# Kernel tuning notes

Hardware: AMD Instinct MI355X
Metric: run time of the kernel (lower is better)

Reference implementation:

```python
import jax, jax.numpy as jnp
import numpy as np

N, C, T, V = 32, 96, 256, 25
S, REL, OUT, BC, KS = 3, 12, 96, 24, 5
DILS = (1, 2)


def setup_inputs() -> dict:
    key = jax.random.key(0)
    ks = jax.random.split(key, 32)
    rn = lambda i, sh, s=1.0: jax.random.normal(ks[i], sh, dtype=jnp.float32) * s
    ru = lambda i, sh: jax.random.uniform(ks[i], sh, dtype=jnp.float32, minval=0.5, maxval=1.5)
    return dict(
        x=rn(0, (N, C, T, V)),
        spd_A=rn(1, (V, V), 0.1),
        A3=rn(2, (S, V, V), 0.1),
        A6=rn(3, (6, V, V), 0.1),
        alpha=jnp.array([0.5], jnp.float32),
        beta=jnp.array([0.5], jnp.float32),
        gamma=jnp.array([0.5], jnp.float32),
        c1_w=rn(4, (S, REL, C), 0.1), c1_b=rn(5, (S, REL), 0.1),
        c2_w=rn(6, (S, REL, C), 0.1), c2_b=rn(7, (S, REL), 0.1),
        c4_w=rn(8, (S, OUT, REL), 0.1), c4_b=rn(9, (S, OUT), 0.1),
        c3_w=rn(10, (S, OUT, C), 0.1), c3_b=rn(11, (S, OUT), 0.1),
        gbn_s=ru(12, (OUT,)), gbn_b=rn(13, (OUT,), 0.1),
        pw_w=rn(14, (4, BC, OUT), 0.1), pw_b=rn(15, (4, BC), 0.1),
        pwbn_s=ru(16, (4, BC)), pwbn_b=rn(17, (4, BC), 0.1),
        tc_w=rn(18, (2, BC, BC, KS), 0.1), tc_b=rn(19, (2, BC), 0.1),
        tcbn_s=ru(20, (2, BC)), tcbn_b=rn(21, (2, BC), 0.1),
        mpbn_s=ru(22, (BC,)), mpbn_b=rn(23, (BC,), 0.1),
    )


def _bn4(h, s, b):  # eval-mode BN folded to per-channel scale/shift, h: [N,C,T,V]
    return h * s[None, :, None, None] + b[None, :, None, None]


def reference(x, spd_A, A3, A6, alpha, beta, gamma,
              c1_w, c1_b, c2_w, c2_b, c4_w, c4_b, c3_w, c3_b,
              gbn_s, gbn_b, pw_w, pw_b, pwbn_s, pwbn_b,
              tc_w, tc_b, tcbn_s, tcbn_b, mpbn_s, mpbn_b):
    # ---- unit_gcn with CTRGC relation modeling ----
    xm = x.mean(axis=2)                                           # [N,C,V] (1x1 conv commutes with T-mean)
    x1 = jnp.einsum('ncv,src->nsrv', xm, c1_w) + c1_b[None, :, :, None]
    x2 = jnp.einsum('ncv,src->nsrv', xm, c2_w) + c2_b[None, :, :, None]
    R = jnp.tanh(x1[..., :, None] - x2[..., None, :])             # [N,S,REL,V,V]
    M = jnp.einsum('nsruv,sor->nsouv', R, c4_w) + c4_b[None, :, :, None, None]
    A6_ex = jnp.tile(A6, (OUT // 6, 1, 1))                        # [OUT,V,V]; A6_ex[c] = A6[c % 6]
    A_at = (M * alpha[0] + A3[None, :, None] + A6_ex[None, None] * beta[0]
            + spd_A * gamma[0])                                   # [N,S,OUT,V,V]
    y = jnp.zeros((N, OUT, T, V), x.dtype)
    for s_ in range(S):
        x3 = jnp.einsum('nctv,oc->notv', x, c3_w[s_]) + c3_b[s_][None, :, None, None]
        y = y + jnp.einsum('nouv,notv->notu', A_at[:, s_], x3)
    y = jax.nn.relu(_bn4(y, gbn_s, gbn_b) + x)                    # residual down = identity (in==out)
    # ---- MultiScale_TemporalConv (internal residual=False) ----
    outs = []
    for b in range(2):  # dilated temporal branches
        h = jax.nn.relu(_bn4(jnp.einsum('nctv,oc->notv', y, pw_w[b])
                             + pw_b[b][None, :, None, None], pwbn_s[b], pwbn_b[b]))
        d = DILS[b]
        pad = 2 * d  # (KS + (KS-1)*(d-1) - 1)//2 for KS=5
        h = jax.lax.conv_general_dilated(
            h, tc_w[b][..., None], window_strides=(1, 1),
            padding=[(pad, pad), (0, 0)], rhs_dilation=(d, 1),
            dimension_numbers=('NCHW', 'OIHW', 'NCHW')) + tc_b[b][None, :, None, None]
        outs.append(_bn4(h, tcbn_s[b], tcbn_b[b]))
    # max-pool branch
    h = jax.nn.relu(_bn4(jnp.einsum('nctv,oc->notv', y, pw_w[2])
                         + pw_b[2][None, :, None, None], pwbn_s[2], pwbn_b[2]))
    h = jax.lax.reduce_window(h, -jnp.inf, jax.lax.max, (1, 1, 3, 1), (1, 1, 1, 1),
                              [(0, 0), (0, 0), (1, 1), (0, 0)])
    outs.append(_bn4(h, mpbn_s, mpbn_b))
    # plain 1x1 branch
    h = jnp.einsum('nctv,oc->notv', y, pw_w[3]) + pw_b[3][None, :, None, None]
    outs.append(_bn4(h, pwbn_s[3], pwbn_b[3]))
    out = jnp.concatenate(outs, axis=1)                           # [N,OUT,T,V]
    return jax.nn.relu(out + x)                                   # outer residual = identity
```

## Files before the change

### kernel.cpp

```cpp
#include <hip/hip_runtime.h>
#include <hip/hip_bf16.h>

typedef __hip_bfloat16 bf16;
typedef __attribute__((ext_vector_type(4))) _Float16 half4;
typedef __attribute__((ext_vector_type(2))) _Float16 half2v;
typedef __attribute__((ext_vector_type(4))) float f32x4;

#define NN 32
#define CC 96
#define TT 256
#define VV 25
#define SS 3
#define RR 12
#define OO 96
#define BCC 24
#define TV (TT*VV)
#define VV2 (VV*VV)

__device__ __forceinline__ float b2f(bf16 v){ return __bfloat162float(v); }
__device__ __forceinline__ bf16  f2b(float v){ return __float2bfloat16(v); }
__device__ __forceinline__ float u2f(unsigned short b){
    union{unsigned u; float f;} a; a.u = ((unsigned)b)<<16; return a.f;
}

__global__ __launch_bounds__(256) void k_mean(const float* __restrict__ x, float* __restrict__ xm)
{
    int idx = blockIdx.x*256 + threadIdx.x;
    if (idx >= NN*CC*VV) return;
    int v  = idx % VV;
    int nc = idx / VV;
    const float* p = x + (size_t)nc*TV + v;
    float s = 0.f;
    for (int t=0;t<TT;t++) s += p[t*VV];
    xm[idx] = s * (1.0f/TT);
}

__global__ __launch_bounds__(256) void k_aat(
    const float* __restrict__ xm,
    const float* __restrict__ c1_w, const float* __restrict__ c1_b,
    const float* __restrict__ c2_w, const float* __restrict__ c2_b,
    const float* __restrict__ c4_w, const float* __restrict__ c4_b,
    const float* __restrict__ A3,  const float* __restrict__ A6, const float* __restrict__ spd,
    const float* __restrict__ alpha, const float* __restrict__ beta, const float* __restrict__ gamma,
    float* __restrict__ Aat)
{
    __shared__ float s_xm[CC*VV];
    __shared__ float s_x1[RR*VV], s_x2[RR*VV];
    __shared__ float s_R[RR*VV2];
    __shared__ float s_c4[OO*RR];
    __shared__ float s_A3[VV2], s_spd[VV2];
    int n = blockIdx.x / SS, s = blockIdx.x % SS;
    int tid = threadIdx.x;
    for (int i=tid;i<CC*VV;i+=256) s_xm[i] = xm[(size_t)n*CC*VV + i];
    for (int i=tid;i<OO*RR;i+=256) s_c4[i] = c4_w[s*OO*RR + i];
    for (int i=tid;i<VV2;i+=256){ s_A3[i]=A3[s*VV2+i]; s_spd[i]=spd[i]; }
    __syncthreads();
    for (int i=tid;i<RR*VV;i+=256){
        int r=i/VV, u=i-r*VV;
        float a1=0.f, a2=0.f;
        for (int c=0;c<CC;c++){
            float xv = s_xm[c*VV+u];
            a1 += c1_w[(s*RR+r)*CC+c]*xv;
            a2 += c2_w[(s*RR+r)*CC+c]*xv;
        }
        s_x1[i]=a1+c1_b[s*RR+r];
        s_x2[i]=a2+c2_b[s*RR+r];
    }
    __syncthreads();
    for (int i=tid;i<RR*VV2;i+=256){
        int r=i/VV2, uv=i-r*VV2, u=uv/VV, v=uv-u*VV;
        s_R[i] = tanhf(s_x1[r*VV+u]-s_x2[r*VV+v]);
    }
    __syncthreads();
    float al=alpha[0], be=beta[0], ga=gamma[0];
    float* op = Aat + ((size_t)n*SS+s)*OO*VV2;
    for (int i=tid;i<OO*VV2;i+=256){
        int o=i/VV2, uv=i-o*VV2;
        float m=0.f;
        #pragma unroll
        for (int r=0;r<RR;r++) m += s_c4[o*RR+r]*s_R[r*VV2+uv];
        m += c4_b[s*OO+o];
        op[i] = m*al + s_A3[uv] + A6[(o%6)*VV2+uv]*be + s_spd[uv]*ga;
    }
}

#define XROW 20
__global__ __launch_bounds__(256,2) void k_gcn(
    const float* __restrict__ x, const float* __restrict__ c3_w, const float* __restrict__ c3_b,
    const float* __restrict__ Aat, const float* __restrict__ gbn_s, const float* __restrict__ gbn_b,
    float* __restrict__ y)
{
    __shared__ __align__(16) _Float16 s_x[800*XROW];
    __shared__ __align__(16) float    s_x3[12*896];
    __shared__ __align__(16) _Float16 s_w[6*16*16];
    __shared__ float s_cb[16];

    int bi  = blockIdx.x;
    int og  = bi % 24;
    int tcb = (bi/24) & 7;
    int n   = bi / 192;
    int t0  = tcb*32;
    int tid = threadIdx.x;

    for (int i=tid;i<16*96;i+=256){
        int m=i/96, c=i-m*96;
        float wf = 0.f;
        if (m<12){ int s=m>>2, op=m&3; wf = c3_w[(s*OO + og*4+op)*CC + c]; }
        s_w[((c>>4)*16+m)*16 + (c&15)] = (_Float16)wf;
    }
    if (tid<16){
        float b=0.f;
        if (tid<12){ int s=tid>>2, op=tid&3; b = c3_b[s*OO + og*4+op]; }
        s_cb[tid]=b;
    }

    int l  = tid & 63;
    int li = l & 15, q = l >> 4;
    int wv_id = tid >> 6;
    int start = wv_id*13;
    int cnt   = (wv_id<3) ? 13 : 11;

    f32x4 acc[13];
    #pragma unroll
    for (int j=0;j<13;++j) acc[j] = (f32x4){0.f,0.f,0.f,0.f};

    size_t xb = (size_t)n*CC*TV + (size_t)t0*VV;
    for (int ck=0; ck<6; ++ck){
        __syncthreads();
        int c0 = ck*16;
        for (int it=0; it<7; ++it){
            int task = tid + it*256;
            if (task < 1600){
                int cpair = task & 7;
                int pq    = task >> 3;
                const float* r0 = x + xb + (size_t)(c0 + cpair*2)*TV + pq*4;
                float4 a = *(const float4*)r0;
                float4 b = *(const float4*)(r0 + TV);
                #pragma unroll
                for (int ii=0; ii<4; ++ii){
                    int p = pq*4 + ii;
                    half2v hv;
                    hv[0] = (_Float16)((&a.x)[ii]);
                    hv[1] = (_Float16)((&b.x)[ii]);
                    *(half2v*)&s_x[p*XROW + cpair*2] = hv;
                }
            }
        }
        __syncthreads();
        half4 a4 = *(const half4*)(s_w + (ck*16+li)*16 + q*4);
        #pragma unroll
        for (int j=0;j<13;++j){
            if (j < cnt){
                half4 b4 = *(const half4*)(s_x + ((start+j)*16 + li)*XROW + q*4);
                acc[j] = __builtin_amdgcn_mfma_f32_16x16x16f16(a4, b4, acc[j], 0, 0, 0);
            }
        }
    }

    if (q < 3){
        #pragma unroll
        for (int j=0;j<13;++j){
            if (j < cnt){
                int p = (start+j)*16 + li;
                int t = p/25, v = p - t*25;
                float* dst = s_x3 + (q*4)*896 + t*28 + v;
                #pragma unroll
                for (int r=0;r<4;++r)
                    dst[r*896] = acc[j][r] + s_cb[q*4+r];
            }
        }
    }
    __syncthreads();

    int w  = wv_id;
    int u  = l & 31;
    int th = l >> 5;
    int o  = og*4 + w;
    int u_eff = (u<VV)?u:(VV-1);
    float areg[75];
    #pragma unroll
    for (int s=0;s<3;s++){
        const float* Ap = Aat + (((size_t)n*SS+s)*OO + o)*VV2 + (size_t)u_eff*VV;
        #pragma unroll
        for (int v=0;v<25;v++) areg[s*25+v] = Ap[v];
    }
    float gs = gbn_s[o], gb = gbn_b[o];
    for (int ti=0; ti<16; ti++){
        int tl = ti*2 + th;
        float a2 = 0.f;
        #pragma unroll
        for (int s=0;s<3;s++){
            const float* xr = &s_x3[(s*4+w)*896 + tl*28];
            #pragma unroll
            for (int vc=0; vc<6; vc++){
                float4 xv4 = *(const float4*)(xr + vc*4);
                a2 += xv4.x*areg[s*25+vc*4]   + xv4.y*areg[s*25+vc*4+1]
                    + xv4.z*areg[s*25+vc*4+2] + xv4.w*areg[s*25+vc*4+3];
            }
            a2 += xr[24]*areg[s*25+24];
        }
        if (u < VV){
            int t = t0 + tl;
            size_t oix = ((size_t)(n*OO+o)*TT + t)*VV + u;
            float yv = gs*a2 + gb + x[oix];
            y[oix] = yv>0.f?yv:0.f;
        }
    }
}

__global__ __launch_bounds__(256,2) void k_pw_h(
    const float* __restrict__ yws, const float* __restrict__ pw_w, const float* __restrict__ pw_b,
    const float* __restrict__ pwbn_s, const float* __restrict__ pwbn_b,
    bf16* __restrict__ h1)
{
    __shared__ __align__(16) float s_w[OO*BCC];
    __shared__ float s_sc[BCC], s_sh[BCC];
    int b   = blockIdx.x/160;
    int rem = blockIdx.x - b*160;
    int n   = rem/5;
    int chunk = rem - (rem/5)*5;
    int pbase = chunk*256 + threadIdx.x;
    for (int i=threadIdx.x;i<OO*BCC;i+=256){
        int o=i/BCC, cp=i-o*BCC;
        s_w[i] = pw_w[(b*BCC+cp)*OO + o];
    }
    if (threadIdx.x<BCC){
        int cp=threadIdx.x;
        float sc = pwbn_s[b*BCC+cp];
        s_sc[cp]=sc;
        s_sh[cp]= sc*pw_b[b*BCC+cp] + pwbn_b[b*BCC+cp];
    }
    __syncthreads();
    float acc[5][BCC];
    #pragma unroll
    for (int j=0;j<5;j++)
        #pragma unroll
        for (int i=0;i<BCC;i++) acc[j][i]=0.f;
    const float* yp = yws + (size_t)n*OO*TV + pbase;
    for (int o=0;o<OO;o++){
        float wv[BCC];
        #pragma unroll
        for (int q=0;q<6;q++) *(float4*)&wv[q*4] = *(const float4*)&s_w[o*BCC + q*4];
        float yv[5];
        #pragma unroll
        for (int j=0;j<5;j++) yv[j] = yp[(size_t)o*TV + j*1280];
        #pragma unroll
        for (int j=0;j<5;j++)
            #pragma unroll
            for (int cp=0;cp<BCC;cp++) acc[j][cp] += wv[cp]*yv[j];
    }
    size_t hb = ((size_t)(b*NN+n)*BCC)*TV + pbase;
    #pragma unroll
    for (int j=0;j<5;j++)
        #pragma unroll
        for (int cp=0;cp<BCC;cp++){
            float h = s_sc[cp]*acc[j][cp] + s_sh[cp];
            h1[hb + (size_t)cp*TV + j*1280] = f2b(h>0.f?h:0.f);
        }
}

__global__ __launch_bounds__(256,2) void k_pw3(
    float* yout, const float* __restrict__ pw_w, const float* __restrict__ pw_b,
    const float* __restrict__ pwbn_s, const float* __restrict__ pwbn_b,
    const float* __restrict__ x)
{
    __shared__ __align__(16) float s_w[OO*BCC];
    __shared__ float s_sc[BCC], s_sh[BCC];
    const int b = 3;
    int n   = blockIdx.x/5;
    int chunk = blockIdx.x - n*5;
    int pbase = chunk*256 + threadIdx.x;
    for (int i=threadIdx.x;i<OO*BCC;i+=256){
        int o=i/BCC, cp=i-o*BCC;
        s_w[i] = pw_w[(b*BCC+cp)*OO + o];
    }
    if (threadIdx.x<BCC){
        int cp=threadIdx.x;
        float sc = pwbn_s[b*BCC+cp];
        s_sc[cp]=sc;
        s_sh[cp]= sc*pw_b[b*BCC+cp] + pwbn_b[b*BCC+cp];
    }
    __syncthreads();
    float acc[5][BCC];
    #pragma unroll
    for (int j=0;j<5;j++)
        #pragma unroll
        for (int i=0;i<BCC;i++) acc[j][i]=0.f;
    const float* yp = yout + (size_t)n*OO*TV + pbase;
    for (int o=0;o<OO;o++){
        float wv[BCC];
        #pragma unroll
        for (int q=0;q<6;q++) *(float4*)&wv[q*4] = *(const float4*)&s_w[o*BCC + q*4];
        float yv[5];
        #pragma unroll
        for (int j=0;j<5;j++) yv[j] = yp[(size_t)o*TV + j*1280];
        #pragma unroll
        for (int j=0;j<5;j++)
            #pragma unroll
            for (int cp=0;cp<BCC;cp++) acc[j][cp] += wv[cp]*yv[j];
    }
    size_t ob = ((size_t)n*OO + 72)*TV + pbase;
    #pragma unroll
    for (int j=0;j<5;j++)
        #pragma unroll
        for (int cp=0;cp<BCC;cp++){
            float h = s_sc[cp]*acc[j][cp] + s_sh[cp];
            size_t ix = ob + (size_t)cp*TV + j*1280;
            float r = h + x[ix];
            yout[ix] = r>0.f?r:0.f;
        }
}

template<int D>
__device__ __forceinline__ void tcn_conv(int n, int br, int t0, int t4, int v, int vv, bool act,
    const float* __restrict__ tc_w, const float* __restrict__ tc_b,
    const float* __restrict__ tcbn_s, const float* __restrict__ tcbn_b,
    const float* __restrict__ x, float* __restrict__ out, const unsigned short* s_h)
{
    const int W = 4 + 4*D;
    int tb = 4 + t4*4 - 2*D;
    for (int g=0; g<4; g++){
        float acc[6][4];
        #pragma unroll
        for (int cpi=0;cpi<6;cpi++)
            #pragma unroll
            for (int i=0;i<4;i++) acc[cpi][i]=0.f;
        for (int ci=0; ci<24; ci++){
            float win[W];
            #pragma unroll
            for (int j=0;j<W;j++) win[j] = u2f(s_h[(ci*40 + tb + j)*26 + vv]);
            #pragma unroll
            for (int cpi=0; cpi<6; cpi++){
                int cp = g*6+cpi;
                const float* wp = tc_w + ((br*BCC+cp)*BCC + ci)*5;
                float w0=wp[0],w1=wp[1],w2=wp[2],w3=wp[3],w4=wp[4];
                #pragma unroll
                for (int i=0;i<4;i++)
                    acc[cpi][i] += w0*win[i] + w1*win[i+D] + w2*win[i+2*D]
                                 + w3*win[i+3*D] + w4*win[i+4*D];
            }
        }
        if (act){
            #pragma unroll
            for (int cpi=0; cpi<6; cpi++){
                int ch = br*BCC + g*6+cpi;
                float tbias=tc_b[ch], ts=tcbn_s[ch], tb2=tcbn_b[ch];
                #pragma unroll
                for (int i=0;i<4;i++){
                    size_t oix = ((size_t)(n*OO+ch)*TT + (t0+t4*4+i))*VV + v;
                    float r = ts*(acc[cpi][i]+tbias) + tb2 + x[oix];
                    out[oix] = r>0.f?r:0.f;
                }
            }
        }
    }
}

__global__ __launch_bounds__(256,2) void k_tcn(
    const bf16* __restrict__ h1, const float* __restrict__ tc_w, const float* __restrict__ tc_b,
    const float* __restrict__ tcbn_s, const float* __restrict__ tcbn_b,
    const float* __restrict__ mpbn_s, const float* __restrict__ mpbn_b,
    const float* __restrict__ x, float* __restrict__ out)
{
    __shared__ unsigned short s_h[24*40*26];
    int bi  = blockIdx.x;
    int n   = bi / 24;
    int rem = bi % 24;
    int br  = rem >> 3;
    int tcb = rem & 7;
    int t0  = tcb*32;
    int tid = threadIdx.x;

    const unsigned short* hb = (const unsigned short*)(h1 + ((size_t)(br*NN+n)*BCC)*TV);
    unsigned short padv = (br==2) ? (unsigned short)0xFF80 : (unsigned short)0;
    for (int ci=0; ci<24; ci++){
        const unsigned short* hc = hb + (size_t)ci*TV;
        #pragma unroll
        for (int j=0;j<5;j++){
            int idx = j*256 + tid;
            if (idx < 1040){
                int tt = idx/26, v = idx - tt*26;
                int gt = t0 - 4 + tt;
                unsigned short bits = padv;
                if (v<25 && gt>=0 && gt<TT) bits = hc[gt*VV+v];
                s_h[(ci*40+tt)*26 + v] = bits;
            }
        }
    }
    __syncthreads();

    int t4 = tid>>5, v = tid&31;
    bool act = v<25;
    int vv = act ? v : 24;

    if (br==0){
        tcn_conv<1>(n,br,t0,t4,v,vv,act,tc_w,tc_b,tcbn_s,tcbn_b,x,out,s_h);
    } else if (br==1){
        tcn_conv<2>(n,br,t0,t4,v,vv,act,tc_w,tc_b,tcbn_s,tcbn_b,x,out,s_h);
    } else {
        int tb = 4 + t4*4 - 1;
        for (int cp=0; cp<24; cp++){
            float win[6];
            #pragma unroll
            for (int j=0;j<6;j++) win[j] = u2f(s_h[(cp*40 + tb + j)*26 + vv]);
            float ms=mpbn_s[cp], mb=mpbn_b[cp];
            if (act){
                #pragma unroll
                for (int i=0;i<4;i++){
                    float m = fmaxf(fmaxf(win[i],win[i+1]),win[i+2]);
                    size_t oix = ((size_t)(n*OO+(48+cp))*TT + (t0+t4*4+i))*VV + v;
                    float r = ms*m + mb + x[oix];
                    out[oix] = r>0.f?r:0.f;
                }
            }
        }
    }
}

extern "C" void kernel_launch(void* const* d_in, const int* in_sizes, int n_in,
                              void* d_out, int out_size, void* d_ws, size_t ws_size,
                              hipStream_t stream)
{
    const float* x     = (const float*)d_in[0];
    const float* spd   = (const float*)d_in[1];
    const float* A3    = (const float*)d_in[2];
    const float* A6    = (const float*)d_in[3];
    const float* alpha = (const float*)d_in[4];
    const float* beta  = (const float*)d_in[5];
    const float* gamma = (const float*)d_in[6];
    const float* c1_w  = (const float*)d_in[7];
    const float* c1_b  = (const float*)d_in[8];
    const float* c2_w  = (const float*)d_in[9];
    const float* c2_b  = (const float*)d_in[10];
    const float* c4_w  = (const float*)d_in[11];
    const float* c4_b  = (const float*)d_in[12];
    const float* c3_w  = (const float*)d_in[13];
    const float* c3_b  = (const float*)d_in[14];
    const float* gbn_s = (const float*)d_in[15];
    const float* gbn_b = (const float*)d_in[16];
    const float* pw_w  = (const float*)d_in[17];
    const float* pw_b  = (const float*)d_in[18];
    const float* pwbn_s= (const float*)d_in[19];
    const float* pwbn_b= (const float*)d_in[20];
    const float* tc_w  = (const float*)d_in[21];
    const float* tc_b  = (const float*)d_in[22];
    const float* tcbn_s= (const float*)d_in[23];
    const float* tcbn_b= (const float*)d_in[24];
    const float* mpbn_s= (const float*)d_in[25];
    const float* mpbn_b= (const float*)d_in[26];
    float* out = (float*)d_out;

    char* ws = (char*)d_ws;
    float* xm  = (float*)(ws);
    float* Aat = (float*)(ws + 307200);
    bf16*  h1  = (bf16*)(ws);

    k_mean<<<dim3(300), dim3(256), 0, stream>>>(x, xm);
    k_aat <<<dim3(96),  dim3(256), 0, stream>>>(xm, c1_w,c1_b,c2_w,c2_b,c4_w,c4_b,
                                                A3, A6, spd, alpha, beta, gamma, Aat);
    k_gcn <<<dim3(6144),dim3(256), 0, stream>>>(x, c3_w, c3_b, Aat, gbn_s, gbn_b, out);
    k_pw_h<<<dim3(480), dim3(256), 0, stream>>>(out, pw_w, pw_b, pwbn_s, pwbn_b, h1);
    k_pw3 <<<dim3(160), dim3(256), 0, stream>>>(out, pw_w, pw_b, pwbn_s, pwbn_b, x);
    k_tcn <<<dim3(768), dim3(256), 0, stream>>>(h1, tc_w, tc_b, tcbn_s, tcbn_b,
                                                mpbn_s, mpbn_b, x, out);
}
```

Before: 846.6 us.

## Move graph aggregation in k_gcn onto fp16 MFMA with half-precision staging

```diff
diff --git a/kernel.cpp b/kernel.cpp
--- a/kernel.cpp
+++ b/kernel.cpp
@@ -84,14 +84,16 @@
     }
 }
 
-#define XROW 20
+#define XROW  20
+#define X3ROW 84
+#define X3OP  (32*X3ROW)
 __global__ __launch_bounds__(256,2) void k_gcn(
     const float* __restrict__ x, const float* __restrict__ c3_w, const float* __restrict__ c3_b,
     const float* __restrict__ Aat, const float* __restrict__ gbn_s, const float* __restrict__ gbn_b,
     float* __restrict__ y)
 {
     __shared__ __align__(16) _Float16 s_x[800*XROW];
-    __shared__ __align__(16) float    s_x3[12*896];
+    __shared__ __align__(16) _Float16 s_x3h[4*X3OP];
     __shared__ __align__(16) _Float16 s_w[6*16*16];
     __shared__ float s_cb[16];
 
@@ -102,6 +104,12 @@
     int t0  = tcb*32;
     int tid = threadIdx.x;
 
+    for (int i=tid; i<4*32*9; i+=256){
+        int op2 = i/288, r2 = i - op2*288;
+        int t = r2/9, kk = 75 + (r2 - t*9);
+        s_x3h[op2*X3OP + t*X3ROW + kk] = (_Float16)0.f;
+    }
+
     for (int i=tid;i<16*96;i+=256){
         int m=i/96, c=i-m*96;
         float wf = 0.f;
@@ -117,6 +125,30 @@
     int l  = tid & 63;
     int li = l & 15, q = l >> 4;
     int wv_id = tid >> 6;
+    int o  = og*4 + wv_id;
+
+    half4 areg[2][5];
+    #pragma unroll
+    for (int mt=0; mt<2; ++mt){
+        int u = mt*16 + li;
+        #pragma unroll
+        for (int kc=0; kc<5; ++kc){
+            half4 h;
+            #pragma unroll
+            for (int e=0; e<4; ++e){
+                int k = kc*16 + q*4 + e;
+                float av = 0.f;
+                if (u < VV && k < 75){
+                    int s = k/25, v = k - s*25;
+                    av = Aat[(((size_t)n*SS+s)*OO + o)*VV2 + u*VV + v];
+                }
+                h[e] = (_Float16)av;
+            }
+            areg[mt][kc] = h;
+        }
+    }
+    float gs = gbn_s[o], gb = gbn_b[o];
+
     int start = wv_id*13;
     int cnt   = (wv_id<3) ? 13 : 11;
 
@@ -156,6 +188,7 @@
             }
         }
     }
+    __syncthreads();
 
     if (q < 3){
         #pragma unroll
@@ -163,47 +196,45 @@
             if (j < cnt){
                 int p = (start+j)*16 + li;
                 int t = p/25, v = p - t*25;
-                float* dst = s_x3 + (q*4)*896 + t*28 + v;
+                int base = t*X3ROW + q*25 + v;
                 #pragma unroll
                 for (int r=0;r<4;++r)
-                    dst[r*896] = acc[j][r] + s_cb[q*4+r];
-            }
-        }
-    }
-    __syncthreads();
-
-    int w  = wv_id;
-    int u  = l & 31;
-    int th = l >> 5;
-    int o  = og*4 + w;
-    int u_eff = (u<VV)?u:(VV-1);
-    float areg[75];
-    #pragma unroll
-    for (int s=0;s<3;s++){
-        const float* Ap = Aat + (((size_t)n*SS+s)*OO + o)*VV2 + (size_t)u_eff*VV;
-        #pragma unroll
-        for (int v=0;v<25;v++) areg[s*25+v] = Ap[v];
-    }
-    float gs = gbn_s[o], gb = gbn_b[o];
-    for (int ti=0; ti<16; ti++){
-        int tl = ti*2 + th;
-        float a2 = 0.f;
-        #pragma unroll
-        for (int s=0;s<3;s++){
-            const float* xr = &s_x3[(s*4+w)*896 + tl*28];
-            #pragma unroll
-            for (int vc=0; vc<6; vc++){
-                float4 xv4 = *(const float4*)(xr + vc*4);
-                a2 += xv4.x*areg[s*25+vc*4]   + xv4.y*areg[s*25+vc*4+1]
-                    + xv4.z*areg[s*25+vc*4+2] + xv4.w*areg[s*25+vc*4+3];
-            }
-            a2 += xr[24]*areg[s*25+24];
-        }
-        if (u < VV){
-            int t = t0 + tl;
-            size_t oix = ((size_t)(n*OO+o)*TT + t)*VV + u;
-            float yv = gs*a2 + gb + x[oix];
-            y[oix] = yv>0.f?yv:0.f;
+                    s_x3h[r*X3OP + base] = (_Float16)(acc[j][r] + s_cb[q*4+r]);
+            }
+        }
+    }
+    __syncthreads();
+
+    const _Float16* bb = s_x3h + wv_id*X3OP;
+    f32x4 acc2[2][2];
+    #pragma unroll
+    for (int mt=0;mt<2;++mt)
+        #pragma unroll
+        for (int nt=0;nt<2;++nt) acc2[mt][nt] = (f32x4){0.f,0.f,0.f,0.f};
+    #pragma unroll
+    for (int kc=0;kc<5;++kc){
+        #pragma unroll
+        for (int nt=0;nt<2;++nt){
+            half4 b4 = *(const half4*)(bb + (nt*16+li)*X3ROW + kc*16 + q*4);
+            #pragma unroll
+            for (int mt=0;mt<2;++mt)
+                acc2[mt][nt] = __builtin_amdgcn_mfma_f32_16x16x16f16(areg[mt][kc], b4, acc2[mt][nt], 0, 0, 0);
+        }
+    }
+    #pragma unroll
+    for (int mt=0;mt<2;++mt){
+        #pragma unroll
+        for (int nt=0;nt<2;++nt){
+            int t = nt*16 + li;
+            #pragma unroll
+            for (int r=0;r<4;++r){
+                int u = mt*16 + q*4 + r;
+                if (u < VV){
+                    size_t oix = ((size_t)(n*OO+o)*TT + (t0+t))*VV + u;
+                    float yv = gs*acc2[mt][nt][r] + gb + x[oix];
+                    y[oix] = yv>0.f?yv:0.f;
+                }
+            }
         }
     }
 }
```

New measurement: 809.5 us. -4.4%, faster.
